# Performance work log

Hardware: AMD Instinct MI355X
Metric: run time of the kernel (lower is better)

The kernel has to match this reference:

```python
import jax, jax.numpy as jnp
import numpy as np
from jax import lax

C = 41  # class_size
B = 1024
T = 1024

def setup_inputs() -> dict:
    key = jax.random.key(0)
    k1, k2, k3, k4 = jax.random.split(key, 4)
    x = jax.random.normal(k1, (B, T, C), dtype=jnp.float32)
    # torchcrf initializes transitions uniform in [-0.1, 0.1]
    start_transitions = jax.random.uniform(k2, (C,), minval=-0.1, maxval=0.1, dtype=jnp.float32)
    end_transitions = jax.random.uniform(k3, (C,), minval=-0.1, maxval=0.1, dtype=jnp.float32)
    transitions = jax.random.uniform(k4, (C, C), minval=-0.1, maxval=0.1, dtype=jnp.float32)
    return {"x": x, "start_transitions": start_transitions,
            "end_transitions": end_transitions, "transitions": transitions}

def reference(x, start_transitions, end_transitions, transitions):
    # Viterbi decode (torchcrf CRF.decode, batch_first, no mask).
    # x: [B, T, C] emissions. Returns best tag sequence [B, T] int32.
    emis_t = jnp.swapaxes(x, 0, 1)  # [T, B, C]
    score0 = start_transitions[None, :] + emis_t[0]  # [B, C]

    def fwd_step(score, emit):
        # score [B, C] (prev tag), emit [B, C] (next tag)
        # next_score[b, i, j] = score[b, i] + trans[i, j] + emit[b, j]
        ns = score[:, :, None] + transitions[None, :, :] + emit[:, None, :]
        best_prev = jnp.argmax(ns, axis=1).astype(jnp.int32)  # [B, C]
        return jnp.max(ns, axis=1), best_prev

    final_score, history = lax.scan(fwd_step, score0, emis_t[1:])  # history [T-1, B, C]
    final_score = final_score + end_transitions[None, :]
    last_tag = jnp.argmax(final_score, axis=1).astype(jnp.int32)  # [B]

    def back_step(tag, idx_t):
        # idx_t [B, C]: best previous tag given current tag
        prev = jnp.take_along_axis(idx_t, tag[:, None], axis=1)[:, 0]
        return prev, prev

    _, tags_prefix = lax.scan(back_step, last_tag, history, reverse=True)  # [T-1, B]
    tags = jnp.concatenate([tags_prefix, last_tag[None, :]], axis=0)  # [T, B]
    return jnp.swapaxes(tags, 0, 1)  # [B, T]
```

## Files before the change

kernel.cpp:

```cpp
#include <hip/hip_runtime.h>
#include <stdint.h>

#define NCLASS 41
#define TLEN   1024
#define NBATCH 1024
#define BP_STRIDE 41944
#define NTRANS (NCLASS * NCLASS)

__device__ __forceinline__ float wave_max_bcast(float x) {
    int xi = __float_as_int(x);
    int t;
    t = __builtin_amdgcn_update_dpp(xi, xi, 0x111, 0xf, 0xf, false);
    x = fmaxf(x, __int_as_float(t)); xi = __float_as_int(x);
    t = __builtin_amdgcn_update_dpp(xi, xi, 0x112, 0xf, 0xf, false);
    x = fmaxf(x, __int_as_float(t)); xi = __float_as_int(x);
    t = __builtin_amdgcn_update_dpp(xi, xi, 0x114, 0xf, 0xf, false);
    x = fmaxf(x, __int_as_float(t)); xi = __float_as_int(x);
    t = __builtin_amdgcn_update_dpp(xi, xi, 0x118, 0xf, 0xf, false);
    x = fmaxf(x, __int_as_float(t)); xi = __float_as_int(x);
    t = __builtin_amdgcn_update_dpp(xi, xi, 0x142, 0xf, 0xf, false);
    x = fmaxf(x, __int_as_float(t)); xi = __float_as_int(x);
    t = __builtin_amdgcn_update_dpp(xi, xi, 0x143, 0xf, 0xf, false);
    x = fmaxf(x, __int_as_float(t));
    return __int_as_float(__builtin_amdgcn_readlane(__float_as_int(x), 63));
}

__global__ __launch_bounds__(64, 1) void crf_forward(
    const float* __restrict__ x,
    const float* __restrict__ start_t,
    const float* __restrict__ end_t,
    const float* __restrict__ trans,
    uint8_t* __restrict__ bp,
    int* __restrict__ out)
{
    __shared__ float tl[NTRANS + 32];

    const int b = blockIdx.x;
    const int j = threadIdx.x;
    const bool act = (j < NCLASS);
    const int jc = act ? j : (NCLASS - 1);

    float mx = -3.0e38f, mn = 3.0e38f;
    for (int k = j; k < NTRANS; k += 64) {
        float v = trans[k];
        tl[k] = v;
        mx = fmaxf(mx, v);
        mn = fminf(mn, v);
    }
    if (j >= NTRANS % 64) {  }
    __syncthreads();
    float Dmax = wave_max_bcast(mx);
    float Dmin = -wave_max_bcast(-mn);
    const float D = Dmax - Dmin;

    const float* xb = x + (size_t)b * TLEN * NCLASS;
    uint8_t* bpb = bp + (size_t)b * BP_STRIDE;

    float score = act ? (start_t[j] + xb[j]) : -3.0e38f;

    auto step = [&](float emit, int t) {
        float M = wave_max_bcast(score);
        float thr = M - D;
        unsigned long long m = __ballot(score >= thr);
        int ic = __ffsll(m) - 1;
        m &= m - 1;
        float sc = __int_as_float(
            __builtin_amdgcn_readlane(__float_as_int(score), ic));
        float best = sc + tl[ic * NCLASS + jc];
        int bidx = ic;
        while (m) {
            ic = __ffsll(m) - 1;
            m &= m - 1;
            sc = __int_as_float(
                __builtin_amdgcn_readlane(__float_as_int(score), ic));
            float vc = sc + tl[ic * NCLASS + jc];
            if (vc > best) { best = vc; bidx = ic; }
        }
        if (act) bpb[(size_t)(t - 1) * NCLASS + j] = (uint8_t)bidx;
        score = act ? (best + emit) : -3.0e38f;
    };

    float e0 = xb[1 * NCLASS + jc];
    float e1 = xb[2 * NCLASS + jc];
    float e2 = xb[3 * NCLASS + jc];
    float e3 = xb[4 * NCLASS + jc];

    int t0 = 1;
    for (; t0 + 3 <= TLEN - 4; t0 += 4) {
        int r0 = t0 + 4, r1 = t0 + 5, r2 = t0 + 6, r3 = t0 + 7;
        r0 = r0 > TLEN - 1 ? TLEN - 1 : r0;
        r1 = r1 > TLEN - 1 ? TLEN - 1 : r1;
        r2 = r2 > TLEN - 1 ? TLEN - 1 : r2;
        r3 = r3 > TLEN - 1 ? TLEN - 1 : r3;
        step(e0, t0 + 0); e0 = xb[(size_t)r0 * NCLASS + jc];
        step(e1, t0 + 1); e1 = xb[(size_t)r1 * NCLASS + jc];
        step(e2, t0 + 2); e2 = xb[(size_t)r2 * NCLASS + jc];
        step(e3, t0 + 3); e3 = xb[(size_t)r3 * NCLASS + jc];
    }
    step(e0, TLEN - 3);
    step(e1, TLEN - 2);
    step(e2, TLEN - 1);

    float fs = act ? (score + end_t[j]) : -3.0e38f;
    int idx = j;
#pragma unroll
    for (int off = 32; off >= 1; off >>= 1) {
        float ov = __shfl_xor(fs, off);
        int oi = __shfl_xor(idx, off);
        if (ov > fs || (ov == fs && oi < idx)) { fs = ov; idx = oi; }
    }
    if (j == 0) out[(size_t)b * TLEN + (TLEN - 1)] = idx;
}

__global__ __launch_bounds__(1024) void crf_backtrack(
    const uint8_t* __restrict__ bp,
    int* __restrict__ out)
{
    __shared__ uint8_t bpl[BP_STRIDE];
    __shared__ int maps[16][NCLASS];
    __shared__ int entry[16];

    const int b = blockIdx.x;
    const int tid = threadIdx.x;
    const int w = tid >> 6;
    const int lane = tid & 63;

    {
        const uint32_t* src = (const uint32_t*)(bp + (size_t)b * BP_STRIDE);
        uint32_t* dst = (uint32_t*)bpl;
        for (int i = tid; i < BP_STRIDE / 4; i += 1024) dst[i] = src[i];
    }
    __syncthreads();

    const int cs = w * 64;
    const int ce = min(cs + 64, TLEN - 1);
    const int L = ce - cs;

    {
        int xx = (lane < NCLASS) ? lane : 0;
        for (int t = ce; t > cs; --t)
            xx = bpl[(t - 1) * NCLASS + xx];
        if (lane < NCLASS) maps[w][lane] = xx;
    }
    __syncthreads();

    if (tid == 0) {
        int cur = out[(size_t)b * TLEN + (TLEN - 1)];
        for (int ww = 15; ww >= 0; --ww) {
            entry[ww] = cur;
            cur = maps[ww][cur];
        }
    }
    __syncthreads();

    {
        int xx = entry[w];
        int cap = 0;
        for (int k = 0; k < L; ++k) {
            xx = bpl[(ce - 1 - k) * NCLASS + xx];
            if (k == lane) cap = xx;
        }
        if (lane < L) out[(size_t)b * TLEN + (ce - 1 - lane)] = cap;
    }
}

extern "C" void kernel_launch(void* const* d_in, const int* in_sizes, int n_in,
                              void* d_out, int out_size, void* d_ws, size_t ws_size,
                              hipStream_t stream) {
    const float* x       = (const float*)d_in[0];
    const float* start_t = (const float*)d_in[1];
    const float* end_t   = (const float*)d_in[2];
    const float* trans   = (const float*)d_in[3];
    int* out = (int*)d_out;
    uint8_t* bp = (uint8_t*)d_ws;

    crf_forward<<<NBATCH, 64, 0, stream>>>(x, start_t, end_t, trans, bp, out);
    crf_backtrack<<<NBATCH, 1024, 0, stream>>>(bp, out);
}
```

Baseline: 255.2 us.

## Predict next-step pruning threshold from bounds to shorten the Viterbi critical path

```diff
diff --git a/kernel.cpp b/kernel.cpp
--- a/kernel.cpp
+++ b/kernel.cpp
@@ -6,6 +6,8 @@
 #define NBATCH 1024
 #define BP_STRIDE 41944
 #define NTRANS (NCLASS * NCLASS)
+#define NEGINF (-3.0e38f)
+#define EPS    2.0e-3f
 
 __device__ __forceinline__ float wave_max_bcast(float x) {
     int xi = __float_as_int(x);
@@ -40,44 +42,60 @@
     const bool act = (j < NCLASS);
     const int jc = act ? j : (NCLASS - 1);
 
-    float mx = -3.0e38f, mn = 3.0e38f;
+    float mx = NEGINF, mn = 3.0e38f;
     for (int k = j; k < NTRANS; k += 64) {
         float v = trans[k];
         tl[k] = v;
         mx = fmaxf(mx, v);
         mn = fminf(mn, v);
     }
-    if (j >= NTRANS % 64) {  }
     __syncthreads();
-    float Dmax = wave_max_bcast(mx);
-    float Dmin = -wave_max_bcast(-mn);
+    const float Dmax = wave_max_bcast(mx);
+    const float Dmin = -wave_max_bcast(-mn);
     const float D = Dmax - Dmin;
+    const float Cc = Dmin - D - EPS;
 
     const float* xb = x + (size_t)b * TLEN * NCLASS;
     uint8_t* bpb = bp + (size_t)b * BP_STRIDE;
 
-    float score = act ? (start_t[j] + xb[j]) : -3.0e38f;
+    float score = act ? (start_t[j] + xb[j]) : NEGINF;
 
-    auto step = [&](float emit, int t) {
-        float M = wave_max_bcast(score);
-        float thr = M - D;
+    float thr = wave_max_bcast(score) - D - EPS;
+
+    auto step = [&](float e, int t) {
         unsigned long long m = __ballot(score >= thr);
-        int ic = __ffsll(m) - 1;
-        m &= m - 1;
-        float sc = __int_as_float(
-            __builtin_amdgcn_readlane(__float_as_int(score), ic));
-        float best = sc + tl[ic * NCLASS + jc];
-        int bidx = ic;
-        while (m) {
-            ic = __ffsll(m) - 1;
-            m &= m - 1;
-            sc = __int_as_float(
+        unsigned long long mb = m & (m - 1);
+        int i1 = __ffsll(m) - 1;
+        int i2 = mb ? (__ffsll(mb) - 1) : i1;
+        unsigned long long m2 = mb & (mb - 1);
+        float s1 = __int_as_float(
+            __builtin_amdgcn_readlane(__float_as_int(score), i1));
+        float s2 = __int_as_float(
+            __builtin_amdgcn_readlane(__float_as_int(score), i2));
+        float t1 = tl[i1 * NCLASS + jc];
+        float t2 = tl[i2 * NCLASS + jc];
+
+        float em = act ? e : NEGINF;
+        float Mt = wave_max_bcast(score);
+        float Et = wave_max_bcast(em);
+        float thrN = Mt + Et + Cc;
+
+        float v1 = s1 + t1;
+        float v2 = s2 + t2;
+        bool c = v2 > v1;
+        float best = c ? v2 : v1;
+        int bidx = c ? i2 : i1;
+        while (m2) {
+            int ic = __ffsll(m2) - 1;
+            m2 &= m2 - 1;
+            float sc = __int_as_float(
                 __builtin_amdgcn_readlane(__float_as_int(score), ic));
             float vc = sc + tl[ic * NCLASS + jc];
             if (vc > best) { best = vc; bidx = ic; }
         }
         if (act) bpb[(size_t)(t - 1) * NCLASS + j] = (uint8_t)bidx;
-        score = act ? (best + emit) : -3.0e38f;
+        score = best + em;
+        thr = thrN;
     };
 
     float e0 = xb[1 * NCLASS + jc];
@@ -101,7 +119,7 @@
     step(e1, TLEN - 2);
     step(e2, TLEN - 1);
 
-    float fs = act ? (score + end_t[j]) : -3.0e38f;
+    float fs = act ? (score + end_t[j]) : NEGINF;
     int idx = j;
 #pragma unroll
     for (int off = 32; off >= 1; off >>= 1) {
```

Result: slower. 357.9 us (+40.3%).

## Predict next-step candidate set from emissions and prefetch transition values

Applied to the files above, without the earlier changes.

```diff
diff --git a/kernel.cpp b/kernel.cpp
--- a/kernel.cpp
+++ b/kernel.cpp
@@ -6,6 +6,7 @@
 #define NBATCH 1024
 #define BP_STRIDE 41944
 #define NTRANS (NCLASS * NCLASS)
+#define NEGINF (-3.0e38f)
 
 __device__ __forceinline__ float wave_max_bcast(float x) {
     int xi = __float_as_int(x);
@@ -24,6 +25,8 @@
     x = fmaxf(x, __int_as_float(t));
     return __int_as_float(__builtin_amdgcn_readlane(__float_as_int(x), 63));
 }
+
+#define RDLANE(v, l) __int_as_float(__builtin_amdgcn_readlane(__float_as_int(v), (l)))
 
 __global__ __launch_bounds__(64, 1) void crf_forward(
     const float* __restrict__ x,
@@ -40,45 +43,87 @@
     const bool act = (j < NCLASS);
     const int jc = act ? j : (NCLASS - 1);
 
-    float mx = -3.0e38f, mn = 3.0e38f;
+    float mx = NEGINF, mn = 3.0e38f;
     for (int k = j; k < NTRANS; k += 64) {
         float v = trans[k];
         tl[k] = v;
         mx = fmaxf(mx, v);
         mn = fminf(mn, v);
     }
-    if (j >= NTRANS % 64) {  }
-    __syncthreads();
-    float Dmax = wave_max_bcast(mx);
-    float Dmin = -wave_max_bcast(-mn);
-    const float D = Dmax - Dmin;
+    __syncthreads();
+    const float Dmax = wave_max_bcast(mx);
+    const float Dmin = -wave_max_bcast(-mn);
+    const float D  = Dmax - Dmin;
+    const float Cc = Dmin - D - 2.0e-3f;
+    const float WP = 2.0f * D + 4.0e-3f;
 
     const float* xb = x + (size_t)b * TLEN * NCLASS;
     uint8_t* bpb = bp + (size_t)b * BP_STRIDE;
 
-    float score = act ? (start_t[j] + xb[j]) : -3.0e38f;
-
-    auto step = [&](float emit, int t) {
-        float M = wave_max_bcast(score);
-        float thr = M - D;
-        unsigned long long m = __ballot(score >= thr);
-        int ic = __ffsll(m) - 1;
-        m &= m - 1;
-        float sc = __int_as_float(
-            __builtin_amdgcn_readlane(__float_as_int(score), ic));
-        float best = sc + tl[ic * NCLASS + jc];
-        int bidx = ic;
-        while (m) {
-            ic = __ffsll(m) - 1;
-            m &= m - 1;
-            sc = __int_as_float(
-                __builtin_amdgcn_readlane(__float_as_int(score), ic));
-            float vc = sc + tl[ic * NCLASS + jc];
-            if (vc > best) { best = vc; bidx = ic; }
-        }
-        if (act) bpb[(size_t)(t - 1) * NCLASS + j] = (uint8_t)bidx;
-        score = act ? (best + emit) : -3.0e38f;
-    };
+    float score = act ? (start_t[j] + xb[j]) : NEGINF;
+
+    float tpA0, tpA1, tpA2, tpA3, thrA; int pA0, pA1, pA2, pA3;
+    unsigned long long mkA;
+    float tpB0, tpB1, tpB2, tpB3, thrB; int pB0, pB1, pB2, pB3;
+    unsigned long long mkB;
+
+#define FILLGEN(G, P_, thv) do {                                              \
+        unsigned long long Pr_ = (P_);                                        \
+        int q0 = __ffsll(Pr_) - 1;            Pr_ &= Pr_ - 1;                 \
+        int q1 = Pr_ ? __ffsll(Pr_) - 1 : q0; Pr_ &= Pr_ - 1;                 \
+        int q2 = Pr_ ? __ffsll(Pr_) - 1 : q1; Pr_ &= Pr_ - 1;                 \
+        int q3 = Pr_ ? __ffsll(Pr_) - 1 : q2;                                 \
+        p##G##0 = q0; p##G##1 = q1; p##G##2 = q2; p##G##3 = q3;               \
+        mk##G = (1ull << q0) | (1ull << q1) | (1ull << q2) | (1ull << q3);    \
+        thr##G = (thv);                                                       \
+        tp##G##0 = tl[q0 * NCLASS + jc];                                      \
+        tp##G##1 = tl[q1 * NCLASS + jc];                                      \
+        tp##G##2 = tl[q2 * NCLASS + jc];                                      \
+        tp##G##3 = tl[q3 * NCLASS + jc];                                      \
+    } while (0)
+
+#define PREP(G, emv) do {                                                     \
+        float E_ = wave_max_bcast(emv);                                       \
+        float M_ = wave_max_bcast(score);                                     \
+        unsigned long long P_ = __ballot((emv) >= E_ - WP);                   \
+        FILLGEN(G, P_, M_ + E_ + Cc);                                         \
+    } while (0)
+
+#define EXEC(G, emv, t) do {                                                  \
+        unsigned long long me = __ballot(score >= thr##G);                    \
+        unsigned long long extra = me & ~mk##G;                               \
+        float s0_ = RDLANE(score, p##G##0);                                   \
+        float s1_ = RDLANE(score, p##G##1);                                   \
+        float s2_ = RDLANE(score, p##G##2);                                   \
+        float s3_ = RDLANE(score, p##G##3);                                   \
+        float v0_ = ((me >> p##G##0) & 1) ? s0_ + tp##G##0 : NEGINF;          \
+        float v1_ = ((me >> p##G##1) & 1) ? s1_ + tp##G##1 : NEGINF;          \
+        float v2_ = ((me >> p##G##2) & 1) ? s2_ + tp##G##2 : NEGINF;          \
+        float v3_ = ((me >> p##G##3) & 1) ? s3_ + tp##G##3 : NEGINF;          \
+        float best = v0_; int bidx = p##G##0;                                 \
+        if (v1_ > best) { best = v1_; bidx = p##G##1; }                       \
+        if (v2_ > best) { best = v2_; bidx = p##G##2; }                       \
+        if (v3_ > best) { best = v3_; bidx = p##G##3; }                       \
+        if (extra) {           \
+            best = NEGINF; bidx = 0;                                          \
+            unsigned long long mm = me;                                       \
+            while (mm) {                                                      \
+                int ic = __ffsll(mm) - 1; mm &= mm - 1;                       \
+                float sc = RDLANE(score, ic);                                 \
+                float vc = sc + tl[ic * NCLASS + jc];                         \
+                if (vc > best) { best = vc; bidx = ic; }                      \
+            }                                                                 \
+        }                                                                     \
+        if (act) bpb[(size_t)((t) - 1) * NCLASS + j] = (uint8_t)bidx;         \
+        score = best + (emv);                                                 \
+    } while (0)
+
+    {
+        float M0 = wave_max_bcast(score);
+        float th1 = M0 - D - 2.0e-3f;
+        unsigned long long P1 = __ballot(score >= th1);
+        FILLGEN(A, P1, th1);
+    }
 
     float e0 = xb[1 * NCLASS + jc];
     float e1 = xb[2 * NCLASS + jc];
@@ -92,16 +137,47 @@
         r1 = r1 > TLEN - 1 ? TLEN - 1 : r1;
         r2 = r2 > TLEN - 1 ? TLEN - 1 : r2;
         r3 = r3 > TLEN - 1 ? TLEN - 1 : r3;
-        step(e0, t0 + 0); e0 = xb[(size_t)r0 * NCLASS + jc];
-        step(e1, t0 + 1); e1 = xb[(size_t)r1 * NCLASS + jc];
-        step(e2, t0 + 2); e2 = xb[(size_t)r2 * NCLASS + jc];
-        step(e3, t0 + 3); e3 = xb[(size_t)r3 * NCLASS + jc];
-    }
-    step(e0, TLEN - 3);
-    step(e1, TLEN - 2);
-    step(e2, TLEN - 1);
-
-    float fs = act ? (score + end_t[j]) : -3.0e38f;
+        {
+            float em = act ? e0 : NEGINF;
+            PREP(B, em);
+            EXEC(A, em, t0 + 0);
+            e0 = xb[(size_t)r0 * NCLASS + jc];
+        }
+        {
+            float em = act ? e1 : NEGINF;
+            PREP(A, em);
+            EXEC(B, em, t0 + 1);
+            e1 = xb[(size_t)r1 * NCLASS + jc];
+        }
+        {
+            float em = act ? e2 : NEGINF;
+            PREP(B, em);
+            EXEC(A, em, t0 + 2);
+            e2 = xb[(size_t)r2 * NCLASS + jc];
+        }
+        {
+            float em = act ? e3 : NEGINF;
+            PREP(A, em);
+            EXEC(B, em, t0 + 3);
+            e3 = xb[(size_t)r3 * NCLASS + jc];
+        }
+    }
+    {
+        float em = act ? e0 : NEGINF;
+        PREP(B, em);
+        EXEC(A, em, TLEN - 3);
+    }
+    {
+        float em = act ? e1 : NEGINF;
+        PREP(A, em);
+        EXEC(B, em, TLEN - 2);
+    }
+    {
+        float em = act ? e2 : NEGINF;
+        EXEC(A, em, TLEN - 1);
+    }
+
+    float fs = act ? (score + end_t[j]) : NEGINF;
     int idx = j;
 #pragma unroll
     for (int off = 32; off >= 1; off >>= 1) {
@@ -110,6 +186,10 @@
         if (ov > fs || (ov == fs && oi < idx)) { fs = ov; idx = oi; }
     }
     if (j == 0) out[(size_t)b * TLEN + (TLEN - 1)] = idx;
+
+#undef FILLGEN
+#undef PREP
+#undef EXEC
 }
 
 __global__ __launch_bounds__(1024) void crf_backtrack(
```

After: 517.0 us. 2.03x slower.
